# Optimization experiments

Measured on AMD Instinct MI355X. Metric: run time of the kernel, lower is better.

## Reference

```python
import jax, jax.numpy as jnp
import numpy as np

B, N, T, F_IN, H, E = 64, 325, 24, 64, 64, 2600
NEG_SLOPE = 0.2


def setup_inputs() -> dict:
    key = jax.random.key(0)
    k1, k2, k3, k4, k5 = jax.random.split(key, 5)
    x = jax.random.normal(k1, (B, N, T, F_IN), dtype=jnp.float32)
    edge_index = jax.random.randint(k2, (2, E), 0, N, dtype=jnp.int32)
    scale = 1.0 / np.sqrt(F_IN)
    W = jax.random.normal(k3, (H, F_IN), dtype=jnp.float32) * scale
    att_src = jax.random.normal(k4, (H,), dtype=jnp.float32) * scale
    att_dst = jax.random.normal(k5, (H,), dtype=jnp.float32) * scale
    bias = jnp.zeros((H,), dtype=jnp.float32)
    return {"x": x, "edge_index": edge_index, "W": W,
            "att_src": att_src, "att_dst": att_dst, "bias": bias}


def reference(x, edge_index, W, att_src, att_dst, bias):
    b, n, t, nf = x.shape
    # Fold the B*T graph replicas into one leading axis: [G, N, F]
    xg = x.transpose(0, 2, 1, 3).reshape(b * t, n, nf)
    h = jnp.einsum('gnf,hf->gnh', xg, W)  # linear transform [G, N, H]
    a_s = h @ att_src  # [G, N] per-node source attention logit
    a_d = h @ att_dst  # [G, N] per-node dest attention logit
    src, dst = edge_index[0], edge_index[1]
    # Per-edge raw score (gather), LeakyReLU as in GATConv: [G, E]
    e = jax.nn.leaky_relu(a_s[:, src] + a_d[:, dst], negative_slope=NEG_SLOPE)

    def per_graph(e_g, h_g):
        # segment softmax over edges grouped by destination node
        m = jax.ops.segment_max(e_g, dst, num_segments=n)
        ex = jnp.exp(e_g - m[dst])
        den = jax.ops.segment_sum(ex, dst, num_segments=n)
        alpha = ex / den[dst]  # [E]
        msg = alpha[:, None] * h_g[src]  # [E, H]
        return jax.ops.segment_sum(msg, dst, num_segments=n)  # [N, H]

    out = jax.vmap(per_graph)(e, h) + bias  # [G, N, H]
    out = jax.nn.gelu(out, approximate=False)
    # Faithful to source: view(B,T,N,H) then raw reshape(B,N,T,H) (row-major reinterpret)
    return out.reshape(b, n, t, -1)
```

## Files before the change

kernel.cpp:

```cpp
#include <hip/hip_runtime.h>
#include <hip/hip_bf16.h>

#define B_  64
#define N_  325
#define T_  24
#define F_  64
#define H_  64
#define E_  2600
#define G_  (B_ * T_)
#define BLK 512
#define GRID3 512

using half2_t = __attribute__((ext_vector_type(2))) _Float16;
using half8_t = __attribute__((ext_vector_type(8))) _Float16;
using f32x4   = __attribute__((ext_vector_type(4))) float;

__global__ __launch_bounds__(512) void k_off_prep(
    const int* __restrict__ ei, const float* __restrict__ W,
    const float* __restrict__ att_src, const float* __restrict__ att_dst,
    int* __restrict__ csr_off, unsigned short* __restrict__ perm,
    float* __restrict__ w_sd) {
  __shared__ int cnt[N_];
  const int tid = threadIdx.x;
  for (int i = tid; i < N_; i += BLK) cnt[i] = 0;
  __syncthreads();
  for (int e = tid; e < E_; e += BLK) atomicAdd(&cnt[ei[E_ + e]], 1);
  __syncthreads();
  if (tid <= N_) {
    int off = 0;
    for (int m = 0; m < N_; ++m) off += (m < tid) ? cnt[m] : 0;
    csr_off[tid] = off;
  }
  if (tid < N_) {
    const int c = cnt[tid];
    int r = 0;
    for (int m = 0; m < N_; ++m) {
      const int cm = cnt[m];
      r += (cm > c || (cm == c && m < tid)) ? 1 : 0;
    }
    perm[r] = (unsigned short)tid;
  }
  if (tid < 128) {
    const int k = tid & 63;
    const float* av = (tid < 64) ? att_src : att_dst;
    float s = 0.f;
    for (int h = 0; h < H_; ++h) s += W[h * F_ + k] * av[h];
    w_sd[tid] = s;
  }
}

__global__ __launch_bounds__(64) void k_scatter(const int* __restrict__ ei,
                                                const int* __restrict__ csr_off,
                                                unsigned short* __restrict__ csr_src) {
  __shared__ int dsts[E_];
  const int tid = threadIdx.x;
  for (int i = tid; i < E_; i += 64) dsts[i] = ei[E_ + i];
  __syncthreads();
  const int e = blockIdx.x * 64 + tid;
  if (e >= E_) return;
  const int myd = dsts[e];
  int rank = 0;
#pragma unroll 4
  for (int k = 0; k < e; ++k) rank += (dsts[k] == myd) ? 1 : 0;
  csr_src[csr_off[myd] + rank] = (unsigned short)ei[e];
}

__device__ __forceinline__ float f16lo(unsigned u) {
  half2_t h = __builtin_bit_cast(half2_t, u); return (float)h[0];
}
__device__ __forceinline__ float f16hi(unsigned u) {
  half2_t h = __builtin_bit_cast(half2_t, u); return (float)h[1];
}
__device__ __forceinline__ unsigned short f16b(float f) {
  _Float16 h = (_Float16)f; return __builtin_bit_cast(unsigned short, h);
}
__device__ __forceinline__ half2_t pkrtz(float a, float b) {
  return __builtin_bit_cast(half2_t, __builtin_amdgcn_cvt_pkrtz(a, b));
}
__device__ __forceinline__ half8_t pk8(float4 a, float4 b) {
  half2_t p0 = pkrtz(a.x, a.y);
  half2_t p1 = pkrtz(a.z, a.w);
  half2_t p2 = pkrtz(b.x, b.y);
  half2_t p3 = pkrtz(b.z, b.w);
  half8_t r;
  r[0] = p0[0]; r[1] = p0[1]; r[2] = p1[0]; r[3] = p1[1];
  r[4] = p2[0]; r[5] = p2[1]; r[6] = p3[0]; r[7] = p3[1];
  return r;
}
__device__ __forceinline__ half8_t ld8f16(const float* p) {
  return pk8(*(const float4*)p, *(const float4*)(p + 4));
}

__device__ __forceinline__ float gelu_f(float v) {
  float t = v * (1.5957691216f + 0.0713550903f * (v * v));
  t = fminf(t, 80.0f);
  float e = __expf(t);
  return v * e * __builtin_amdgcn_rcpf(e + 1.0f);
}

__global__ __launch_bounds__(512, 4) void k_gat3(
    const float* __restrict__ x, const int* __restrict__ csr_off_g,
    const unsigned short* __restrict__ csr_src_g,
    const unsigned short* __restrict__ perm_g, const float* __restrict__ W,
    const float* __restrict__ w_sd, const float* __restrict__ bias,
    float* __restrict__ out) {
  __shared__ _Float16 h_s[N_][H_];
  __shared__ unsigned pack_s[E_];
  __shared__ unsigned short edst_s[E_];
  __shared__ unsigned asad_s[N_];
  __shared__ float den_s[N_];
  __shared__ unsigned short coff_s[N_ + 1];
  __shared__ unsigned short perm_s[N_];

  const int tid  = threadIdx.x;
  const int lane = tid & 63;
  const int wv   = tid >> 6;
  const int l15  = lane & 15;
  const int l4   = lane >> 4;

  for (int i = tid; i < E_; i += BLK) pack_s[i] = (unsigned)csr_src_g[i];
  for (int i = tid; i <= N_; i += BLK) coff_s[i] = csr_off_g[i];
  for (int i = tid; i < N_; i += BLK) perm_s[i] = perm_g[i];
  __syncthreads();
  if (tid < N_) {
    const int b = coff_s[tid], e2 = coff_s[tid + 1];
    for (int p = b; p < e2; ++p) edst_s[p] = (unsigned short)tid;
  }

  half8_t bf[2][4];
#pragma unroll
  for (int ct = 0; ct < 4; ++ct)
#pragma unroll
    for (int k0 = 0; k0 < 2; ++k0)
      bf[k0][ct] = ld8f16(W + (size_t)(ct * 16 + l15) * F_ + k0 * 32 + l4 * 8);

  half8_t bw[2];
  {
    const float* wp = w_sd + (l15 & 1) * 64;
#pragma unroll
    for (int k0 = 0; k0 < 2; ++k0) {
      half8_t z = {0, 0, 0, 0, 0, 0, 0, 0};
      bw[k0] = (l15 < 2) ? ld8f16(wp + k0 * 32 + l4 * 8) : z;
    }
  }

  const int l16v = tid & 15;
  const int qw   = tid >> 4;
  const float4 bias4 = *(const float4*)(bias + 4 * l16v);

  for (int gi = 0; gi < 3; ++gi) {
    const int g  = blockIdx.x + (gi << 9);
    const int bb = g / T_;
    const int tt = g % T_;
    if (gi) __syncthreads();

    const float* xg = x + ((size_t)bb * N_ * T_ + tt) * F_;
    for (int t = wv; t < 21; t += 8) {
      const int r0 = t * 16;
      int rr = r0 + l15; if (rr > N_ - 1) rr = N_ - 1;
      const float* xr = xg + (size_t)rr * (T_ * F_);
      const float4 u0 = *(const float4*)(xr + l4 * 8);
      const float4 u1 = *(const float4*)(xr + l4 * 8 + 4);
      const float4 u2 = *(const float4*)(xr + 32 + l4 * 8);
      const float4 u3 = *(const float4*)(xr + 32 + l4 * 8 + 4);
      const half8_t a0 = pk8(u0, u1);
      const half8_t a1 = pk8(u2, u3);
      const bool full = (r0 + 16 <= N_);

#pragma unroll
      for (int ct = 0; ct < 4; ++ct) {
        f32x4 acc = {0.f, 0.f, 0.f, 0.f};
        acc = __builtin_amdgcn_mfma_f32_16x16x32_f16(a0, bf[0][ct], acc, 0, 0, 0);
        acc = __builtin_amdgcn_mfma_f32_16x16x32_f16(a1, bf[1][ct], acc, 0, 0, 0);
        const int col = ct * 16 + l15;
#pragma unroll
        for (int j = 0; j < 4; ++j) {
          const int row = r0 + l4 * 4 + j;
          if (full || row < N_) h_s[row][col] = (_Float16)acc[j];
        }
      }
      f32x4 acc2 = {0.f, 0.f, 0.f, 0.f};
      acc2 = __builtin_amdgcn_mfma_f32_16x16x32_f16(a0, bw[0], acc2, 0, 0, 0);
      acc2 = __builtin_amdgcn_mfma_f32_16x16x32_f16(a1, bw[1], acc2, 0, 0, 0);
      if (l15 < 2) {
#pragma unroll
        for (int j = 0; j < 4; ++j) {
          const int row = r0 + l4 * 4 + j;
          if (full || row < N_)
            ((unsigned short*)asad_s)[row * 2 + l15] = f16b(acc2[j]);
        }
      }
    }
    __syncthreads();

    for (int p = tid; p < E_; p += BLK) {
      const unsigned u = pack_s[p];
      const unsigned sp = u & 0xffffu;
      const unsigned dp = edst_s[p];
      float e = f16lo(asad_s[sp]) + f16hi(asad_s[dp]);
      e = fmaxf(e, 0.2f * e);
      const float ex = __expf(e - 5.0f);
      pack_s[p] = sp | ((unsigned)f16b(ex) << 16);
    }
    __syncthreads();

    if (tid < N_) {
      const int n = perm_s[tid];
      const int beg = coff_s[n], end = coff_s[n + 1];
      float den = 0.f;
      for (int p = beg; p < end; ++p) den += f16hi(pack_s[p]);
      den_s[n] = (end > beg) ? (1.0f / den) : 1.0f;
    }
    __syncthreads();

    for (int idx = qw; idx < N_; idx += 32) {
      const int n = perm_s[idx];
      const int beg = coff_s[n], end = coff_s[n + 1];
      half2_t a01 = {(_Float16)0.f, (_Float16)0.f};
      half2_t a23 = {(_Float16)0.f, (_Float16)0.f};
      for (int p = beg; p < end; ++p) {
        const unsigned u  = pack_s[p];
        const unsigned s  = u & 0xffffu;
        const unsigned au = u >> 16;
        const half2_t al2 = __builtin_bit_cast(half2_t, au | (au << 16));
        const uint2 hv = *(const uint2*)&h_s[s][4 * l16v];
        a01 = al2 * __builtin_bit_cast(half2_t, hv.x) + a01;
        a23 = al2 * __builtin_bit_cast(half2_t, hv.y) + a23;
      }
      const float inv = den_s[n];
      const float v0 = gelu_f((float)a01[0] * inv + bias4.x);
      const float v1 = gelu_f((float)a01[1] * inv + bias4.y);
      const float v2 = gelu_f((float)a23[0] * inv + bias4.z);
      const float v3 = gelu_f((float)a23[1] * inv + bias4.w);
      *(float4*)&out[((size_t)g * N_ + n) * H_ + 4 * l16v] =
          make_float4(v0, v1, v2, v3);
    }
  }
}

extern "C" void kernel_launch(void* const* d_in, const int* in_sizes, int n_in,
                              void* d_out, int out_size, void* d_ws, size_t ws_size,
                              hipStream_t stream) {
  (void)in_sizes; (void)n_in; (void)out_size; (void)ws_size;
  const float* x       = (const float*)d_in[0];
  const int*   ei      = (const int*)d_in[1];
  const float* W       = (const float*)d_in[2];
  const float* att_src = (const float*)d_in[3];
  const float* att_dst = (const float*)d_in[4];
  const float* bias    = (const float*)d_in[5];
  float* out = (float*)d_out;

  char* ws = (char*)d_ws;
  int*            csr_off = (int*)(ws + 0);
  unsigned short* csr_src = (unsigned short*)(ws + 4096);
  unsigned short* perm    = (unsigned short*)(ws + 16384);
  float*          w_sd    = (float*)(ws + 20480);

  k_off_prep<<<1, BLK, 0, stream>>>(ei, W, att_src, att_dst, csr_off, perm, w_sd);
  k_scatter<<<(E_ + 63) / 64, 64, 0, stream>>>(ei, csr_off, csr_src);
  k_gat3<<<GRID3, BLK, 0, stream>>>(x, csr_off, csr_src, perm, W, w_sd, bias, out);
}
```

Measured before the change: 123.7 us.

## Prefetch next graph's x tiles into registers and fuse edge-score with denominator pass

Each block now loads the x rows for the next graph replica into registers while it runs the MFMA projection for the current one, so global load latency overlaps with compute. The per-edge exp pass and the per-node denominator pass are merged into one per-destination loop, which removes the edst_s array and one block barrier per graph. The h_s row stride is padded to 68 halves to reduce LDS bank conflicts in the aggregation gather. In exchange the prefetch buffers add 48 floats of registers per thread, which may reduce occupancy. The fused loop also gives only one thread per destination node to the edge work, so parallelism there drops, especially for high-degree nodes.

```diff
diff --git a/kernel.cpp b/kernel.cpp
--- a/kernel.cpp
+++ b/kernel.cpp
@@ -10,6 +10,7 @@
 #define G_  (B_ * T_)
 #define BLK 512
 #define GRID3 512
+#define HS  68
 
 using half2_t = __attribute__((ext_vector_type(2))) _Float16;
 using half8_t = __attribute__((ext_vector_type(8))) _Float16;
@@ -87,9 +88,6 @@
   r[4] = p2[0]; r[5] = p2[1]; r[6] = p3[0]; r[7] = p3[1];
   return r;
 }
-__device__ __forceinline__ half8_t ld8f16(const float* p) {
-  return pk8(*(const float4*)p, *(const float4*)(p + 4));
-}
 
 __device__ __forceinline__ float gelu_f(float v) {
   float t = v * (1.5957691216f + 0.0713550903f * (v * v));
@@ -104,9 +102,8 @@
     const unsigned short* __restrict__ perm_g, const float* __restrict__ W,
     const float* __restrict__ w_sd, const float* __restrict__ bias,
     float* __restrict__ out) {
-  __shared__ _Float16 h_s[N_][H_];
+  __shared__ _Float16 h_s[N_][HS];
   __shared__ unsigned pack_s[E_];
-  __shared__ unsigned short edst_s[E_];
   __shared__ unsigned asad_s[N_];
   __shared__ float den_s[N_];
   __shared__ unsigned short coff_s[N_ + 1];
@@ -118,21 +115,37 @@
   const int l15  = lane & 15;
   const int l4   = lane >> 4;
 
+  float4 xa[3][4];
+#define LOAD_TILE(GI2, TI)                                                      \
+  {                                                                             \
+    const int t_ = wv + (TI) * 8;                                               \
+    if (t_ < 21) {                                                              \
+      const int g2_ = blockIdx.x + ((GI2) << 9);                                \
+      const int bb_ = g2_ / T_, tt_ = g2_ % T_;                                 \
+      int rr_ = t_ * 16 + l15; if (rr_ > N_ - 1) rr_ = N_ - 1;                  \
+      const float* xr_ = x + ((size_t)bb_ * N_ * T_ + tt_) * F_ +               \
+                         (size_t)rr_ * (T_ * F_) + l4 * 8;                      \
+      xa[TI][0] = *(const float4*)xr_;                                          \
+      xa[TI][1] = *(const float4*)(xr_ + 4);                                    \
+      xa[TI][2] = *(const float4*)(xr_ + 32);                                   \
+      xa[TI][3] = *(const float4*)(xr_ + 36);                                   \
+    }                                                                           \
+  }
+
+  LOAD_TILE(0, 0) LOAD_TILE(0, 1) LOAD_TILE(0, 2)
+
   for (int i = tid; i < E_; i += BLK) pack_s[i] = (unsigned)csr_src_g[i];
   for (int i = tid; i <= N_; i += BLK) coff_s[i] = csr_off_g[i];
   for (int i = tid; i < N_; i += BLK) perm_s[i] = perm_g[i];
-  __syncthreads();
-  if (tid < N_) {
-    const int b = coff_s[tid], e2 = coff_s[tid + 1];
-    for (int p = b; p < e2; ++p) edst_s[p] = (unsigned short)tid;
-  }
 
   half8_t bf[2][4];
 #pragma unroll
   for (int ct = 0; ct < 4; ++ct)
 #pragma unroll
-    for (int k0 = 0; k0 < 2; ++k0)
-      bf[k0][ct] = ld8f16(W + (size_t)(ct * 16 + l15) * F_ + k0 * 32 + l4 * 8);
+    for (int k0 = 0; k0 < 2; ++k0) {
+      const float* p = W + (size_t)(ct * 16 + l15) * F_ + k0 * 32 + l4 * 8;
+      bf[k0][ct] = pk8(*(const float4*)p, *(const float4*)(p + 4));
+    }
 
   half8_t bw[2];
   {
@@ -140,9 +153,11 @@
 #pragma unroll
     for (int k0 = 0; k0 < 2; ++k0) {
       half8_t z = {0, 0, 0, 0, 0, 0, 0, 0};
-      bw[k0] = (l15 < 2) ? ld8f16(wp + k0 * 32 + l4 * 8) : z;
-    }
-  }
+      const float* p = wp + k0 * 32 + l4 * 8;
+      bw[k0] = (l15 < 2) ? pk8(*(const float4*)p, *(const float4*)(p + 4)) : z;
+    }
+  }
+  __syncthreads();
 
   const int l16v = tid & 15;
   const int qw   = tid >> 4;
@@ -150,65 +165,61 @@
 
   for (int gi = 0; gi < 3; ++gi) {
     const int g  = blockIdx.x + (gi << 9);
-    const int bb = g / T_;
-    const int tt = g % T_;
     if (gi) __syncthreads();
 
-    const float* xg = x + ((size_t)bb * N_ * T_ + tt) * F_;
-    for (int t = wv; t < 21; t += 8) {
-      const int r0 = t * 16;
-      int rr = r0 + l15; if (rr > N_ - 1) rr = N_ - 1;
-      const float* xr = xg + (size_t)rr * (T_ * F_);
-      const float4 u0 = *(const float4*)(xr + l4 * 8);
-      const float4 u1 = *(const float4*)(xr + l4 * 8 + 4);
-      const float4 u2 = *(const float4*)(xr + 32 + l4 * 8);
-      const float4 u3 = *(const float4*)(xr + 32 + l4 * 8 + 4);
-      const half8_t a0 = pk8(u0, u1);
-      const half8_t a1 = pk8(u2, u3);
-      const bool full = (r0 + 16 <= N_);
-
-#pragma unroll
-      for (int ct = 0; ct < 4; ++ct) {
-        f32x4 acc = {0.f, 0.f, 0.f, 0.f};
-        acc = __builtin_amdgcn_mfma_f32_16x16x32_f16(a0, bf[0][ct], acc, 0, 0, 0);
-        acc = __builtin_amdgcn_mfma_f32_16x16x32_f16(a1, bf[1][ct], acc, 0, 0, 0);
-        const int col = ct * 16 + l15;
-#pragma unroll
-        for (int j = 0; j < 4; ++j) {
-          const int row = r0 + l4 * 4 + j;
-          if (full || row < N_) h_s[row][col] = (_Float16)acc[j];
+#pragma unroll
+    for (int ti = 0; ti < 3; ++ti) {
+      const int t = wv + ti * 8;
+      if (t < 21) {
+        const int r0 = t * 16;
+        const half8_t a0 = pk8(xa[ti][0], xa[ti][1]);
+        const half8_t a1 = pk8(xa[ti][2], xa[ti][3]);
+        if (gi < 2) {
+          if (ti == 0) LOAD_TILE(gi + 1, 0)
+          if (ti == 1) LOAD_TILE(gi + 1, 1)
+          if (ti == 2) LOAD_TILE(gi + 1, 2)
+        }
+        const bool full = (r0 + 16 <= N_);
+#pragma unroll
+        for (int ct = 0; ct < 4; ++ct) {
+          f32x4 acc = {0.f, 0.f, 0.f, 0.f};
+          acc = __builtin_amdgcn_mfma_f32_16x16x32_f16(a0, bf[0][ct], acc, 0, 0, 0);
+          acc = __builtin_amdgcn_mfma_f32_16x16x32_f16(a1, bf[1][ct], acc, 0, 0, 0);
+          const int col = ct * 16 + l15;
+#pragma unroll
+          for (int j = 0; j < 4; ++j) {
+            const int row = r0 + l4 * 4 + j;
+            if (full || row < N_) h_s[row][col] = (_Float16)acc[j];
+          }
+        }
+        f32x4 acc2 = {0.f, 0.f, 0.f, 0.f};
+        acc2 = __builtin_amdgcn_mfma_f32_16x16x32_f16(a0, bw[0], acc2, 0, 0, 0);
+        acc2 = __builtin_amdgcn_mfma_f32_16x16x32_f16(a1, bw[1], acc2, 0, 0, 0);
+        if (l15 < 2) {
+#pragma unroll
+          for (int j = 0; j < 4; ++j) {
+            const int row = r0 + l4 * 4 + j;
+            if (full || row < N_)
+              ((unsigned short*)asad_s)[row * 2 + l15] = f16b(acc2[j]);
+          }
         }
       }
-      f32x4 acc2 = {0.f, 0.f, 0.f, 0.f};
-      acc2 = __builtin_amdgcn_mfma_f32_16x16x32_f16(a0, bw[0], acc2, 0, 0, 0);
-      acc2 = __builtin_amdgcn_mfma_f32_16x16x32_f16(a1, bw[1], acc2, 0, 0, 0);
-      if (l15 < 2) {
-#pragma unroll
-        for (int j = 0; j < 4; ++j) {
-          const int row = r0 + l4 * 4 + j;
-          if (full || row < N_)
-            ((unsigned short*)asad_s)[row * 2 + l15] = f16b(acc2[j]);
-        }
+    }
+    __syncthreads();
+
+    if (tid < N_) {
+      const int n   = perm_s[tid];
+      const int beg = coff_s[n], end = coff_s[n + 1];
+      const float adn = f16hi(asad_s[n]);
+      float den = 0.f;
+      for (int p = beg; p < end; ++p) {
+        const unsigned sp = pack_s[p] & 0xffffu;
+        float e = f16lo(asad_s[sp]) + adn;
+        e = fmaxf(e, 0.2f * e);
+        const float ex = __expf(e - 5.0f);
+        den += ex;
+        pack_s[p] = sp | ((unsigned)f16b(ex) << 16);
       }
-    }
-    __syncthreads();
-
-    for (int p = tid; p < E_; p += BLK) {
-      const unsigned u = pack_s[p];
-      const unsigned sp = u & 0xffffu;
-      const unsigned dp = edst_s[p];
-      float e = f16lo(asad_s[sp]) + f16hi(asad_s[dp]);
-      e = fmaxf(e, 0.2f * e);
-      const float ex = __expf(e - 5.0f);
-      pack_s[p] = sp | ((unsigned)f16b(ex) << 16);
-    }
-    __syncthreads();
-
-    if (tid < N_) {
-      const int n = perm_s[tid];
-      const int beg = coff_s[n], end = coff_s[n + 1];
-      float den = 0.f;
-      for (int p = beg; p < end; ++p) den += f16hi(pack_s[p]);
       den_s[n] = (end > beg) ? (1.0f / den) : 1.0f;
     }
     __syncthreads();
@@ -236,6 +247,7 @@
           make_float4(v0, v1, v2, v3);
     }
   }
+#undef LOAD_TILE
 }
 
 extern "C" void kernel_launch(void* const* d_in, const int* in_sizes, int n_in,
```

Result: slower. 136.2 us (+10.1%).
